# Kernel tuning notes

Hardware: AMD Instinct MI355X
Metric: run time of the kernel (lower is better)

Reference implementation:

```python
import jax, jax.numpy as jnp
import numpy as np

N, E, D, L, H = 100000, 1600000, 64, 4, 4
C = D // H  # head dim = 16
NEG_SLOPE = 0.2


def layer_norm(x, g, b, eps=1e-5):
    m = jnp.mean(x, axis=-1, keepdims=True)
    v = jnp.var(x, axis=-1, keepdims=True)
    return (x - m) * jax.lax.rsqrt(v + eps) * g + b


def setup_inputs() -> dict:
    key = jax.random.key(0)
    ks = jax.random.split(key, 12)
    node_feats = jax.random.normal(ks[0], (N, D), jnp.float32)
    edge_feats = jax.random.normal(ks[1], (E, D), jnp.float32)
    edge_index = jax.random.randint(ks[2], (2, E), 0, N, jnp.int32)
    s = 0.1
    conv_w = jax.random.normal(ks[3], (L, D, H * C), jnp.float32) * s
    att_src = jax.random.normal(ks[4], (L, H, C), jnp.float32) * s
    att_dst = jax.random.normal(ks[5], (L, H, C), jnp.float32) * s
    edge_w = jax.random.normal(ks[6], (L, D, H * C), jnp.float32) * s
    att_edge = jax.random.normal(ks[7], (L, H, C), jnp.float32) * s
    conv_b = jnp.zeros((L, D), jnp.float32)
    ln_g = jnp.ones((L, D), jnp.float32)
    ln_b = jnp.zeros((L, D), jnp.float32)
    Din = 3 * D  # edge-update MLP input dim (node_i, node_j, edge)
    up1_w = jax.random.normal(ks[8], (L, Din, Din), jnp.float32) * 0.05
    up1_b = jnp.zeros((L, Din), jnp.float32)
    up_ln_g = jnp.ones((L, Din), jnp.float32)
    up_ln_b = jnp.zeros((L, Din), jnp.float32)
    up2_w = jax.random.normal(ks[9], (L, Din, D), jnp.float32) * 0.05
    up2_b = jnp.zeros((L, D), jnp.float32)
    return dict(node_feats=node_feats, edge_feats=edge_feats, edge_index=edge_index,
                conv_w=conv_w, att_src=att_src, att_dst=att_dst, edge_w=edge_w,
                att_edge=att_edge, conv_b=conv_b, ln_g=ln_g, ln_b=ln_b,
                up1_w=up1_w, up1_b=up1_b, up_ln_g=up_ln_g, up_ln_b=up_ln_b,
                up2_w=up2_w, up2_b=up2_b)


def _gat_conv(x, e, src, dst, w, a_s, a_d, ew, a_e, b):
    n = x.shape[0]
    # add self loops with zero edge attr
    loop = jnp.arange(n, dtype=src.dtype)
    src_f = jnp.concatenate([src, loop])
    dst_f = jnp.concatenate([dst, loop])
    xh = (x @ w).reshape(n, H, C)                       # [N,H,C]
    alpha_src = jnp.einsum('nhc,hc->nh', xh, a_s)        # [N,H]
    alpha_dst = jnp.einsum('nhc,hc->nh', xh, a_d)
    eh = (e @ ew).reshape(-1, H, C)                      # [E,H,C]
    alpha_edge = jnp.einsum('ehc,hc->eh', eh, a_e)       # [E,H]
    alpha_edge = jnp.concatenate([alpha_edge, jnp.zeros((n, H), x.dtype)])
    alpha = alpha_src[src_f] + alpha_dst[dst_f] + alpha_edge  # [E+N,H]
    alpha = jax.nn.leaky_relu(alpha, NEG_SLOPE)
    # segment softmax over destination neighborhoods
    amax = jax.ops.segment_max(alpha, dst_f, num_segments=n)
    alpha = jnp.exp(alpha - amax[dst_f])
    asum = jax.ops.segment_sum(alpha, dst_f, num_segments=n)
    alpha = alpha / (asum[dst_f] + 1e-16)
    msg = xh[src_f] * alpha[:, :, None]                  # [E+N,H,C]
    out = jax.ops.segment_sum(msg.reshape(-1, H * C), dst_f, num_segments=n)
    return out + b


def _edge_update(nf, ef, src, dst, w1, b1, g, bg, w2, b2):
    x = jnp.concatenate([nf[src], nf[dst], ef], axis=-1)  # [E,3D]
    h = layer_norm(x @ w1 + b1, g, bg)
    h = jax.nn.relu(h)
    return h @ w2 + b2 + ef


def reference(node_feats, edge_feats, edge_index, conv_w, att_src, att_dst,
              edge_w, att_edge, conv_b, ln_g, ln_b, up1_w, up1_b,
              up_ln_g, up_ln_b, up2_w, up2_b):
    src, dst = edge_index[0], edge_index[1]
    nf, ef = node_feats, edge_feats
    for l in range(L):
        conv = _gat_conv(nf, ef, src, dst, conv_w[l], att_src[l], att_dst[l],
                         edge_w[l], att_edge[l], conv_b[l])
        conv = layer_norm(conv, ln_g[l], ln_b[l])
        nf = jax.nn.relu(conv) + nf  # dropout in eval mode = identity
        ef = _edge_update(nf, ef, src, dst, up1_w[l], up1_b[l],
                          up_ln_g[l], up_ln_b[l], up2_w[l], up2_b[l])
    return nf, ef
```

## Files before the change

### kernel.cpp

```cpp
#include <hip/hip_runtime.h>
#include <math.h>

#define NN 100000
#define NE 1600000
#define DD 64
#define NL 4
#define NH 4
#define NC 16
#define DIN 192
#define SLOPE 0.2f
#define EB 64
#define XSTR 200
#define FSTR 66
#define RSTR 68
#define LOG2E 1.44269504088896340736f

typedef __bf16 bf8 __attribute__((ext_vector_type(8)));
typedef __bf16 bf4 __attribute__((ext_vector_type(4)));
typedef __bf16 bf2 __attribute__((ext_vector_type(2)));
typedef float f32x4 __attribute__((ext_vector_type(4)));

__device__ __forceinline__ f32x4 MFMA(bf8 a, bf8 b, f32x4 c) {
  return __builtin_amdgcn_mfma_f32_16x16x32_bf16(a, b, c, 0, 0, 0);
}

__global__ void k_pack_w1(const float* __restrict__ W1, __bf16* __restrict__ WH) {
  int gidx = blockIdx.x * 256 + threadIdx.x;
  if (gidx >= 4 * 4608) return;
  int lyr = gidx / 4608, rem = gidx % 4608;
  int lane = rem & 63, ts = rem >> 6;
  int s = ts % 6, t = ts / 6;
  const float* Wl = W1 + (size_t)lyr * DIN * DIN;
  size_t base = (size_t)lyr * 36864 + ((size_t)(t * 6 + s) * 64 + lane) * 8;
  int k0 = s * 32 + (lane >> 4) * 8, n = t * 16 + (lane & 15);
#pragma unroll
  for (int j = 0; j < 8; ++j)
    WH[base + j] = (__bf16)Wl[(size_t)(k0 + j) * DIN + n];
}

__global__ void k_pack_w2(const float* __restrict__ W2, __bf16* __restrict__ WH) {
  int gidx = blockIdx.x * 256 + threadIdx.x;
  if (gidx >= 4 * 1536) return;
  int lyr = gidx / 1536, rem = gidx % 1536;
  int lane = rem & 63, ts = rem >> 6;
  int s = ts % 6, t = ts / 6;
  const float* Wl = W2 + (size_t)lyr * DIN * DD;
  size_t base = (size_t)lyr * 12288 + ((size_t)(t * 6 + s) * 64 + lane) * 8;
  int k0 = s * 32 + (lane >> 4) * 8, n = t * 16 + (lane & 15);
#pragma unroll
  for (int j = 0; j < 8; ++j)
    WH[base + j] = (__bf16)Wl[(size_t)(k0 + j) * DD + n];
}

__global__ void k_w2v(const float* __restrict__ up2_w, const float* __restrict__ up2_b,
                      const float* __restrict__ vbuf, __bf16* __restrict__ W2VP,
                      __bf16* __restrict__ VP, float* __restrict__ bvdot) {
  int l = blockIdx.x;
  const float* vn = vbuf + (l + 1) * 256;
  int t = threadIdx.x;
  if (t < 384) {
    int s = t >> 6, lane = t & 63;
    int i = lane & 15, k0 = s * 32 + (lane >> 4) * 8;
    const float* W2 = up2_w + (size_t)l * DIN * DD;
    __bf16* out = W2VP + (size_t)l * 3072 + ((size_t)(s * 64 + lane)) * 8;
#pragma unroll
    for (int j = 0; j < 8; ++j) {
      float val = 0.f;
      if (i < 4)
        for (int n = 0; n < DD; ++n)
          val = fmaf(W2[(size_t)(k0 + j) * DD + n], vn[n * NH + i], val);
      out[j] = (__bf16)val;
    }
  }
  if (t < 128) {
    int s2 = t >> 6, lane = t & 63;
    int i = lane & 15, k0 = s2 * 32 + (lane >> 4) * 8;
    __bf16* out = VP + (size_t)l * 1024 + ((size_t)(s2 * 64 + lane)) * 8;
#pragma unroll
    for (int j = 0; j < 8; ++j)
      out[j] = (i < 4) ? (__bf16)vn[(k0 + j) * NH + i] : (__bf16)0.f;
  }
  if (t < 4) {
    const float* b2 = up2_b + (size_t)l * DD;
    float bv = 0.f;
    for (int n = 0; n < DD; ++n) bv = fmaf(b2[n], vn[n * NH + t], bv);
    bvdot[l * 4 + t] = bv;
  }
}

__global__ void k_zero(int* __restrict__ deg) {
  int i = blockIdx.x * 256 + threadIdx.x;
  if (i < NN) deg[i] = 0;
}

__global__ void k_hist(const int* __restrict__ dst, int* __restrict__ deg) {
  int e = blockIdx.x * 256 + threadIdx.x;
  if (e < NE) atomicAdd(&deg[dst[e]], 1);
}

__global__ void k_scan1(const int* __restrict__ deg, int* __restrict__ offs,
                        int* __restrict__ bsum) {
  __shared__ int sh[256];
  int t = threadIdx.x, b = blockIdx.x;
  int i0 = b * 1024 + t * 4;
  int d0 = (i0 + 0 < NN) ? deg[i0 + 0] : 0;
  int d1 = (i0 + 1 < NN) ? deg[i0 + 1] : 0;
  int d2 = (i0 + 2 < NN) ? deg[i0 + 2] : 0;
  int d3 = (i0 + 3 < NN) ? deg[i0 + 3] : 0;
  int s4 = d0 + d1 + d2 + d3;
  sh[t] = s4;
  __syncthreads();
  int p = 0;
#pragma unroll
  for (int off = 1; off < 256; off <<= 1) {
    int v = (t >= off) ? sh[t - off] : 0;
    __syncthreads();
    sh[t] += v;
    __syncthreads();
  }
  p = sh[t] - s4;
  if (t == 255) bsum[b] = sh[255];
  if (i0 + 0 < NN) offs[i0 + 0] = p;
  if (i0 + 1 < NN) offs[i0 + 1] = p + d0;
  if (i0 + 2 < NN) offs[i0 + 2] = p + d0 + d1;
  if (i0 + 3 < NN) offs[i0 + 3] = p + d0 + d1 + d2;
}

__global__ void k_scan2(int* __restrict__ bsum, int* __restrict__ boff,
                        int* __restrict__ offs, int nb) {
  if (threadIdx.x == 0 && blockIdx.x == 0) {
    int run = 0;
    for (int k = 0; k < nb; ++k) { boff[k] = run; run += bsum[k]; }
    offs[NN] = NE;
  }
}

__global__ void k_scan3(int* __restrict__ offs, const int* __restrict__ boff,
                        int* __restrict__ cursor) {
  int i = blockIdx.x * 256 + threadIdx.x;
  if (i < NN) {
    int v = offs[i] + boff[i >> 10];
    offs[i] = v;
    cursor[i] = v;
  }
}

__global__ void k_scatter(const int* __restrict__ src, const int* __restrict__ dst,
                          int* __restrict__ cursor, int* __restrict__ csr_src,
                          int* __restrict__ csr_eid) {
  int e = blockIdx.x * 256 + threadIdx.x;
  if (e >= NE) return;
  int pos = atomicAdd(&cursor[dst[e]], 1);
  csr_src[pos] = src[e];
  csr_eid[pos] = e;
}

__global__ void k_v_all(const float* __restrict__ ew_all, const float* __restrict__ ae_all,
                        float* __restrict__ vbuf) {
  int l = blockIdx.x;
  const float* ew = ew_all + (size_t)l * DD * DD;
  const float* ae = ae_all + (size_t)l * NH * NC;
  int d = threadIdx.x >> 2, h = threadIdx.x & 3;
  float s = 0.f;
#pragma unroll
  for (int c = 0; c < NC; ++c) s = fmaf(ew[d * DD + h * NC + c], ae[h * NC + c], s);
  vbuf[l * 256 + d * NH + h] = s;
}

__global__ void k_init_nf(const float* __restrict__ node_feats, float* __restrict__ nf) {
  int i = blockIdx.x * 256 + threadIdx.x;
  if (i < NN * DD) nf[i] = node_feats[i];
}

__global__ void k_xh(const float* __restrict__ nf, const float* __restrict__ W,
                     const float* __restrict__ as_, const float* __restrict__ ad_,
                     __bf16* __restrict__ xh16, float* __restrict__ asrc,
                     float* __restrict__ adst) {
  int t = blockIdx.x * 4 + (threadIdx.x >> 6);
  int d = threadIdx.x & 63;
  if (t >= NN) return;
  const float* x = nf + (size_t)t * DD;
  float acc = 0.f;
#pragma unroll
  for (int k = 0; k < DD; ++k) acc = fmaf(x[k], W[k * DD + d], acc);
  xh16[(size_t)t * DD + d] = (__bf16)acc;
  int h = d >> 4, c = d & 15;
  float ps = acc * as_[h * NC + c];
  float pd = acc * ad_[h * NC + c];
#pragma unroll
  for (int off = 8; off >= 1; off >>= 1) {
    ps += __shfl_xor(ps, off, 64);
    pd += __shfl_xor(pd, off, 64);
  }
  if (c == 0) { asrc[t * NH + h] = ps; adst[t * NH + h] = pd; }
}

__global__ void k_pass1f(const float* __restrict__ edge_feats,
                         const float* __restrict__ v,
                         __bf16* __restrict__ ef16, float* __restrict__ araw) {
  int e = blockIdx.x * 64 + (threadIdx.x >> 2);
  int part = threadIdx.x & 3;
  if (e >= NE) return;
  float ph0 = 0.f, ph1 = 0.f, ph2 = 0.f, ph3 = 0.f;
  const float4* ep = (const float4*)(edge_feats + (size_t)e * DD + part * 16);
  const float4* v4 = (const float4*)v;
  bf4 outv[4];
#pragma unroll
  for (int c4 = 0; c4 < 4; ++c4) {
    float4 x = ep[c4];
    outv[c4][0] = (__bf16)x.x; outv[c4][1] = (__bf16)x.y;
    outv[c4][2] = (__bf16)x.z; outv[c4][3] = (__bf16)x.w;
    int d0 = part * 16 + c4 * 4;
    float4 va = v4[d0], vb = v4[d0 + 1], vc = v4[d0 + 2], vd = v4[d0 + 3];
    ph0 = fmaf(x.x, va.x, fmaf(x.y, vb.x, fmaf(x.z, vc.x, fmaf(x.w, vd.x, ph0))));
    ph1 = fmaf(x.x, va.y, fmaf(x.y, vb.y, fmaf(x.z, vc.y, fmaf(x.w, vd.y, ph1))));
    ph2 = fmaf(x.x, va.z, fmaf(x.y, vb.z, fmaf(x.z, vc.z, fmaf(x.w, vd.z, ph2))));
    ph3 = fmaf(x.x, va.w, fmaf(x.y, vb.w, fmaf(x.z, vc.w, fmaf(x.w, vd.w, ph3))));
  }
  *(bf8*)&ef16[(size_t)e * DD + part * 16] =
      (bf8){outv[0][0], outv[0][1], outv[0][2], outv[0][3],
            outv[1][0], outv[1][1], outv[1][2], outv[1][3]};
  *(bf8*)&ef16[(size_t)e * DD + part * 16 + 8] =
      (bf8){outv[2][0], outv[2][1], outv[2][2], outv[2][3],
            outv[3][0], outv[3][1], outv[3][2], outv[3][3]};
#pragma unroll
  for (int off = 1; off <= 2; off <<= 1) {
    ph0 += __shfl_xor(ph0, off, 64);
    ph1 += __shfl_xor(ph1, off, 64);
    ph2 += __shfl_xor(ph2, off, 64);
    ph3 += __shfl_xor(ph3, off, 64);
  }
  float pe = (part == 0) ? ph0 : (part == 1) ? ph1 : (part == 2) ? ph2 : ph3;
  araw[(size_t)e * NH + part] = pe;
}

__global__ __launch_bounds__(256) void k_gather3(
    const __bf16* __restrict__ xh16, const float* __restrict__ araw,
    const int* __restrict__ csr_src, const int* __restrict__ csr_eid,
    const int* __restrict__ offs,
    const float* __restrict__ asrc, const float* __restrict__ adst,
    const float* __restrict__ cb, const float* __restrict__ g,
    const float* __restrict__ bln, float* __restrict__ nf,
    __bf16* __restrict__ nf16) {
  int t = blockIdx.x * 4 + (threadIdx.x >> 6);
  int d = threadIdx.x & 63;
  if (t >= NN) return;
  int h = d >> 4;
  int o0 = offs[t], o1 = offs[t + 1];
  int deg = o1 - o0;
  float adh = adst[t * NH + h];

  float sh = asrc[t * NH + h] + adh;
  sh = ((sh > 0.f) ? sh : SLOPE * sh) * LOG2E;
  float m_run = sh;
  float wsum = 1.f;
  float acc = (float)xh16[(size_t)t * DD + d];

  int j = 0;
  for (; j + 1 < deg; j += 2) {
    int pos0 = o0 + j, pos1 = o0 + j + 1;
    int sp0 = csr_src[pos0], sp1 = csr_src[pos1];
    int e0i = csr_eid[pos0], e1i = csr_eid[pos1];
    float ar0 = asrc[sp0 * NH + h] + adh + araw[(size_t)e0i * NH + h];
    float ar1 = asrc[sp1 * NH + h] + adh + araw[(size_t)e1i * NH + h];
    ar0 = ((ar0 > 0.f) ? ar0 : SLOPE * ar0) * LOG2E;
    ar1 = ((ar1 > 0.f) ? ar1 : SLOPE * ar1) * LOG2E;
    float x0 = (float)xh16[(size_t)sp0 * DD + d];
    float x1 = (float)xh16[(size_t)sp1 * DD + d];
    float mnew = fmaxf(m_run, fmaxf(ar0, ar1));
    float rold = exp2f(m_run - mnew);
    float w0 = exp2f(ar0 - mnew), w1 = exp2f(ar1 - mnew);
    acc = fmaf(w1, x1, fmaf(w0, x0, acc * rold));
    wsum = fmaf(w0 + w1, 1.f, wsum * rold);
    m_run = mnew;
  }
  if (j < deg) {
    int pos = o0 + j;
    int sp = csr_src[pos];
    int ei = csr_eid[pos];
    float ar = asrc[sp * NH + h] + adh + araw[(size_t)ei * NH + h];
    ar = ((ar > 0.f) ? ar : SLOPE * ar) * LOG2E;
    float xv = (float)xh16[(size_t)sp * DD + d];
    float mnew = fmaxf(m_run, ar);
    float rold = exp2f(m_run - mnew);
    float w = exp2f(ar - mnew);
    acc = fmaf(w, xv, acc * rold);
    wsum = fmaf(w, 1.f, wsum * rold);
    m_run = mnew;
  }

  float val = acc / (wsum + 1e-16f) + cb[d];
  float m = val;
#pragma unroll
  for (int off = 32; off >= 1; off >>= 1) m += __shfl_xor(m, off, 64);
  m *= (1.f / 64.f);
  float c = val - m;
  float q = c * c;
#pragma unroll
  for (int off = 32; off >= 1; off >>= 1) q += __shfl_xor(q, off, 64);
  float rstd = 1.f / sqrtf(q * (1.f / 64.f) + 1e-5f);
  float y = c * rstd * g[d] + bln[d];
  y = fmaxf(y, 0.f);
  float out = y + nf[(size_t)t * DD + d];
  nf[(size_t)t * DD + d] = out;
  nf16[(size_t)t * DD + d] = (__bf16)out;
}

__global__ __launch_bounds__(256, 4) void k_edge_mlp15(
    const __bf16* __restrict__ nf16, __bf16* __restrict__ ef16,
    float* __restrict__ efout,
    const int* __restrict__ src, const int* __restrict__ dst,
    const __bf16* __restrict__ W1H, const float* __restrict__ b1,
    const float* __restrict__ g, const float* __restrict__ bg,
    const __bf16* __restrict__ W2H, const float* __restrict__ b2,
    const __bf16* __restrict__ W2VP, const __bf16* __restrict__ VP,
    const float* __restrict__ bvdot, float* __restrict__ araw, int last) {
  __shared__ __bf16 XH[EB * XSTR];
  __shared__ __bf16 RESB[EB * RSTR];
  __shared__ __bf16 Pb[EB * 8];
  int tid = threadIdx.x;
  int e0 = blockIdx.x * EB;
  float* XF = (float*)XH;

  {
    int row = tid >> 2, p = tid & 3;
    int se = src[e0 + row], de = dst[e0 + row];
    const bf8* psrc = (const bf8*)(nf16 + (size_t)se * DD + p * 16);
    *(bf8*)&XH[row * XSTR + p * 16]     = psrc[0];
    *(bf8*)&XH[row * XSTR + p * 16 + 8] = psrc[1];
    const bf8* pdst = (const bf8*)(nf16 + (size_t)de * DD + p * 16);
    *(bf8*)&XH[row * XSTR + 64 + p * 16]     = pdst[0];
    *(bf8*)&XH[row * XSTR + 64 + p * 16 + 8] = pdst[1];
    const bf8* pef = (const bf8*)(ef16 + (size_t)(e0 + row) * DD + p * 16);
    bf8 ev0 = pef[0], ev1 = pef[1];
    *(bf8*)&XH[row * XSTR + 128 + p * 16]     = ev0;
    *(bf8*)&XH[row * XSTR + 128 + p * 16 + 8] = ev1;
    *(bf8*)&RESB[row * RSTR + p * 16]     = ev0;
    *(bf8*)&RESB[row * RSTR + p * 16 + 8] = ev1;
  }
  __syncthreads();

  int cg = tid >> 6, l = tid & 63;
  int gq = l >> 4, i = l & 15;
  int col = cg * 16 + i;

  f32x4 acc[4][3];
#pragma unroll
  for (int rt = 0; rt < 4; ++rt)
#pragma unroll
    for (int t = 0; t < 3; ++t) acc[rt][t] = (f32x4){0.f, 0.f, 0.f, 0.f};
  f32x4 accP = (f32x4){0.f, 0.f, 0.f, 0.f};
  f32x4 accQ = (f32x4){0.f, 0.f, 0.f, 0.f};

#pragma unroll
  for (int s = 0; s < 6; ++s) {
    bf8 a[4];
#pragma unroll
    for (int rt = 0; rt < 4; ++rt)
      a[rt] = *(const bf8*)&XH[(rt * 16 + i) * XSTR + s * 32 + gq * 8];
#pragma unroll
    for (int t = 0; t < 3; ++t) {
      bf8 bh = *(const bf8*)(W1H + ((size_t)((cg * 3 + t) * 6 + s) * 64 + l) * 8);
#pragma unroll
      for (int rt = 0; rt < 4; ++rt) acc[rt][t] = MFMA(a[rt], bh, acc[rt][t]);
    }
    if (!last && s >= 4) {
      bf8 acg = *(const bf8*)&XH[(cg * 16 + i) * XSTR + s * 32 + gq * 8];
      bf8 vp = *(const bf8*)(VP + ((size_t)((s - 4) * 64 + l)) * 8);
      accP = MFMA(acg, vp, accP);
    }
  }

  float b1v[3], gv[3], bgv[3];
#pragma unroll
  for (int t = 0; t < 3; ++t) {
    int n = cg * 48 + t * 16 + i;
    b1v[t] = b1[n]; gv[t] = g[n]; bgv[t] = bg[n];
  }
#pragma unroll
  for (int rt = 0; rt < 4; ++rt)
#pragma unroll
    for (int t = 0; t < 3; ++t)
#pragma unroll
      for (int r = 0; r < 4; ++r) acc[rt][t][r] += b1v[t];

#pragma unroll
  for (int rt = 0; rt < 4; ++rt)
#pragma unroll
    for (int r = 0; r < 4; ++r) {
      float sm = 0.f, sq = 0.f;
#pragma unroll
      for (int t = 0; t < 3; ++t) { float x = acc[rt][t][r]; sm += x; sq = fmaf(x, x, sq); }
#pragma unroll
      for (int off = 1; off <= 8; off <<= 1) {
        sm += __shfl_xor(sm, off, 64);
        sq += __shfl_xor(sq, off, 64);
      }
      if (i == 0) {
        int row = rt * 16 + gq * 4 + r;
        bf2 pr; pr[0] = (__bf16)sm; pr[1] = (__bf16)sq;
        *(bf2*)&Pb[row * 8 + cg * 2] = pr;
      }
    }
  __syncthreads();

  if (tid < EB) {
    bf8 pv = *(const bf8*)&Pb[tid * 8];
    float sm = (float)pv[0] + (float)pv[2] + (float)pv[4] + (float)pv[6];
    float sq = (float)pv[1] + (float)pv[3] + (float)pv[5] + (float)pv[7];
    float mean = sm * (1.f / (float)DIN);
    float var = sq * (1.f / (float)DIN) - mean * mean;
    float rstd = 1.f / sqrtf(var + 1e-5f);
    bf2 mv; mv[0] = (__bf16)mean; mv[1] = (__bf16)rstd;
    *(bf2*)&Pb[tid * 8] = mv;
  }
  __syncthreads();

#pragma unroll
  for (int rt = 0; rt < 4; ++rt)
#pragma unroll
    for (int r = 0; r < 4; ++r) {
      int row = rt * 16 + gq * 4 + r;
      bf2 mv = *(const bf2*)&Pb[row * 8];
      float mean = (float)mv[0], rstd = (float)mv[1];
#pragma unroll
      for (int t = 0; t < 3; ++t) {
        float y = (acc[rt][t][r] - mean) * rstd * gv[t] + bgv[t];
        y = fmaxf(y, 0.f);
        XH[row * XSTR + cg * 48 + t * 16 + i] = (__bf16)y;
      }
    }
  __syncthreads();

  f32x4 acc2[4];
#pragma unroll
  for (int rt = 0; rt < 4; ++rt) acc2[rt] = (f32x4){0.f, 0.f, 0.f, 0.f};

#pragma unroll
  for (int s = 0; s < 6; ++s) {
    bf8 a2[4];
#pragma unroll
    for (int rt = 0; rt < 4; ++rt)
      a2[rt] = *(const bf8*)&XH[(rt * 16 + i) * XSTR + s * 32 + gq * 8];
    bf8 bh = *(const bf8*)(W2H + ((size_t)(cg * 6 + s) * 64 + l) * 8);
#pragma unroll
    for (int rt = 0; rt < 4; ++rt) acc2[rt] = MFMA(a2[rt], bh, acc2[rt]);
    if (!last) {
      bf8 acg = *(const bf8*)&XH[(cg * 16 + i) * XSTR + s * 32 + gq * 8];
      bf8 wv = *(const bf8*)(W2VP + ((size_t)(s * 64 + l)) * 8);
      accQ = MFMA(acg, wv, accQ);
    }
  }
  __syncthreads();

  float b2v = b2[col];
#pragma unroll
  for (int rt = 0; rt < 4; ++rt)
#pragma unroll
    for (int r = 0; r < 4; ++r) {
      int row = rt * 16 + gq * 4 + r;
      float resv = (float)RESB[row * RSTR + col];
      XF[row * FSTR + col] = acc2[rt][r] + b2v + resv;
    }

  if (!last && i < 4) {
    float bvd = bvdot[i];
#pragma unroll
    for (int r = 0; r < 4; ++r) {
      int row = cg * 16 + gq * 4 + r;
      araw[(size_t)(e0 + row) * NH + i] = accP[r] + accQ[r] + bvd;
    }
  }
  __syncthreads();

  {
    int row = tid >> 2, q = tid & 3;
    const float* fr = &XF[row * FSTR + q * 16];
    if (last) {
      float* op = efout + (size_t)(e0 + row) * DD + q * 16;
#pragma unroll
      for (int k = 0; k < 4; ++k)
        *(float4*)(op + k * 4) = *(const float4*)(fr + k * 4);
    } else {
      bf8 o0, o1;
#pragma unroll
      for (int k = 0; k < 8; ++k) { o0[k] = (__bf16)fr[k]; o1[k] = (__bf16)fr[k + 8]; }
      __bf16* op = ef16 + (size_t)(e0 + row) * DD + q * 16;
      *(bf8*)op = o0;
      *(bf8*)(op + 8) = o1;
    }
  }
}

extern "C" void kernel_launch(void* const* d_in, const int* in_sizes, int n_in,
                              void* d_out, int out_size, void* d_ws, size_t ws_size,
                              hipStream_t stream) {
  const float* node_feats = (const float*)d_in[0];
  const float* edge_feats = (const float*)d_in[1];
  const int*   edge_index = (const int*)d_in[2];
  const float* conv_w  = (const float*)d_in[3];
  const float* att_src = (const float*)d_in[4];
  const float* att_dst = (const float*)d_in[5];
  const float* edge_w  = (const float*)d_in[6];
  const float* att_edge= (const float*)d_in[7];
  const float* conv_b  = (const float*)d_in[8];
  const float* ln_g    = (const float*)d_in[9];
  const float* ln_b    = (const float*)d_in[10];
  const float* up1_w   = (const float*)d_in[11];
  const float* up1_b   = (const float*)d_in[12];
  const float* up_ln_g = (const float*)d_in[13];
  const float* up_ln_b = (const float*)d_in[14];
  const float* up2_w   = (const float*)d_in[15];
  const float* up2_b   = (const float*)d_in[16];

  const int* src = edge_index;
  const int* dst = edge_index + NE;

  float* nf = (float*)d_out;
  float* efout = nf + (size_t)NN * DD;

  float* w = (float*)d_ws;
  __bf16* xh16 = (__bf16*)w; w += (size_t)NN * DD / 2;
  __bf16* nf16 = (__bf16*)w; w += (size_t)NN * DD / 2;
  __bf16* ef16 = (__bf16*)w; w += (size_t)NE * DD / 2;
  float* asrc  = w; w += (size_t)NN * NH;
  float* adst  = w; w += (size_t)NN * NH;
  float* araw  = w; w += (size_t)NE * NH;
  float* vbuf  = w; w += 4 * 256;
  float* bvdot = w; w += 16;
  __bf16* W1H  = (__bf16*)w; w += (size_t)4 * 36864 / 2;
  __bf16* W2H  = (__bf16*)w; w += (size_t)4 * 12288 / 2;
  __bf16* W2VP = (__bf16*)w; w += (size_t)3 * 3072 / 2;
  __bf16* VPb  = (__bf16*)w; w += (size_t)3 * 1024 / 2;
  int* deg     = (int*)w; w += NN;
  int* offs    = (int*)w; w += NN + 1;
  int* cursor  = (int*)w; w += NN;
  int* bsum    = (int*)w; w += 128;
  int* boff    = (int*)w; w += 128;
  int* csr_src = (int*)w; w += NE;
  int* csr_eid = (int*)w; w += NE;

  k_init_nf<<<(NN * DD + 255) / 256, 256, 0, stream>>>(node_feats, nf);
  k_pack_w1<<<72, 256, 0, stream>>>(up1_w, W1H);
  k_pack_w2<<<24, 256, 0, stream>>>(up2_w, W2H);

  const int nb = (NN + 1023) / 1024;
  k_zero<<<(NN + 255) / 256, 256, 0, stream>>>(deg);
  k_hist<<<(NE + 255) / 256, 256, 0, stream>>>(dst, deg);
  k_scan1<<<nb, 256, 0, stream>>>(deg, offs, bsum);
  k_scan2<<<1, 64, 0, stream>>>(bsum, boff, offs, nb);
  k_scan3<<<(NN + 255) / 256, 256, 0, stream>>>(offs, boff, cursor);
  k_scatter<<<(NE + 255) / 256, 256, 0, stream>>>(src, dst, cursor, csr_src, csr_eid);

  k_v_all<<<4, 256, 0, stream>>>(edge_w, att_edge, vbuf);
  k_w2v<<<3, 384, 0, stream>>>(up2_w, up2_b, vbuf, W2VP, VPb, bvdot);
  k_pass1f<<<NE / 64, 256, 0, stream>>>(edge_feats, vbuf, ef16, araw);

  for (int l = 0; l < NL; ++l) {
    int last = (l == NL - 1) ? 1 : 0;
    k_xh<<<NN / 4, 256, 0, stream>>>(nf, conv_w + (size_t)l * DD * DD,
                                     att_src + (size_t)l * NH * NC,
                                     att_dst + (size_t)l * NH * NC, xh16, asrc, adst);
    k_gather3<<<NN / 4, 256, 0, stream>>>(xh16, araw, csr_src, csr_eid, offs,
                                          asrc, adst,
                                          conv_b + (size_t)l * DD,
                                          ln_g + (size_t)l * DD,
                                          ln_b + (size_t)l * DD, nf, nf16);
    k_edge_mlp15<<<NE / EB, 256, 0, stream>>>(
        nf16, ef16, efout, src, dst,
        W1H + (size_t)l * 36864, up1_b + (size_t)l * DIN,
        up_ln_g + (size_t)l * DIN, up_ln_b + (size_t)l * DIN,
        W2H + (size_t)l * 12288, up2_b + (size_t)l * DD,
        last ? W2VP : (W2VP + (size_t)l * 3072),
        last ? VPb : (VPb + (size_t)l * 1024),
        bvdot + (size_t)l * 4, araw, last);
  }
}
```

Before: 2.789 ms.

## Fuse next-layer node projection into gather kernel, keep node residual in bf16

Removes the separate per-layer k_xh launch by computing the next layer's projection, xh and attention logits at the end of the gather kernel. The input row is broadcast across lanes with shuffles, and xh and the attention buffers are double-buffered across layers. The fp32 node-feature copy and init kernel are dropped: the residual is now carried in bf16 and fp32 is written only on the last layer. This saves node-feature traffic and launches, at the cost of bf16 rounding accumulating in the residual across layers.

```diff
diff --git a/kernel.cpp b/kernel.cpp
--- a/kernel.cpp
+++ b/kernel.cpp
@@ -167,19 +167,15 @@
   vbuf[l * 256 + d * NH + h] = s;
 }
 
-__global__ void k_init_nf(const float* __restrict__ node_feats, float* __restrict__ nf) {
-  int i = blockIdx.x * 256 + threadIdx.x;
-  if (i < NN * DD) nf[i] = node_feats[i];
-}
-
-__global__ void k_xh(const float* __restrict__ nf, const float* __restrict__ W,
-                     const float* __restrict__ as_, const float* __restrict__ ad_,
-                     __bf16* __restrict__ xh16, float* __restrict__ asrc,
-                     float* __restrict__ adst) {
+__global__ void k_xh0(const float* __restrict__ node_feats, const float* __restrict__ W,
+                      const float* __restrict__ as_, const float* __restrict__ ad_,
+                      __bf16* __restrict__ nf16, __bf16* __restrict__ xh16,
+                      float* __restrict__ asrc, float* __restrict__ adst) {
   int t = blockIdx.x * 4 + (threadIdx.x >> 6);
   int d = threadIdx.x & 63;
   if (t >= NN) return;
-  const float* x = nf + (size_t)t * DD;
+  const float* x = node_feats + (size_t)t * DD;
+  nf16[(size_t)t * DD + d] = (__bf16)x[d];
   float acc = 0.f;
 #pragma unroll
   for (int k = 0; k < DD; ++k) acc = fmaf(x[k], W[k * DD + d], acc);
@@ -234,14 +230,17 @@
   araw[(size_t)e * NH + part] = pe;
 }
 
-__global__ __launch_bounds__(256) void k_gather3(
+__global__ __launch_bounds__(256) void k_gather4(
     const __bf16* __restrict__ xh16, const float* __restrict__ araw,
     const int* __restrict__ csr_src, const int* __restrict__ csr_eid,
     const int* __restrict__ offs,
     const float* __restrict__ asrc, const float* __restrict__ adst,
     const float* __restrict__ cb, const float* __restrict__ g,
-    const float* __restrict__ bln, float* __restrict__ nf,
-    __bf16* __restrict__ nf16) {
+    const float* __restrict__ bln, __bf16* __restrict__ nf16,
+    float* __restrict__ nfout,
+    const float* __restrict__ Wn, const float* __restrict__ asn,
+    const float* __restrict__ adn, __bf16* __restrict__ xh16n,
+    float* __restrict__ asrcn, float* __restrict__ adstn, int last) {
   int t = blockIdx.x * 4 + (threadIdx.x >> 6);
   int d = threadIdx.x & 63;
   if (t >= NN) return;
@@ -301,9 +300,29 @@
   float rstd = 1.f / sqrtf(q * (1.f / 64.f) + 1e-5f);
   float y = c * rstd * g[d] + bln[d];
   y = fmaxf(y, 0.f);
-  float out = y + nf[(size_t)t * DD + d];
-  nf[(size_t)t * DD + d] = out;
+  float out = y + (float)nf16[(size_t)t * DD + d];
   nf16[(size_t)t * DD + d] = (__bf16)out;
+
+  if (last) {
+    nfout[(size_t)t * DD + d] = out;
+  } else {
+    float acc2 = 0.f;
+#pragma unroll 8
+    for (int k = 0; k < DD; ++k) {
+      float xk = __shfl(out, k, 64);
+      acc2 = fmaf(xk, Wn[k * DD + d], acc2);
+    }
+    xh16n[(size_t)t * DD + d] = (__bf16)acc2;
+    int cc = d & 15;
+    float ps = acc2 * asn[h * NC + cc];
+    float pd = acc2 * adn[h * NC + cc];
+#pragma unroll
+    for (int off = 8; off >= 1; off >>= 1) {
+      ps += __shfl_xor(ps, off, 64);
+      pd += __shfl_xor(pd, off, 64);
+    }
+    if (cc == 0) { asrcn[t * NH + h] = ps; adstn[t * NH + h] = pd; }
+  }
 }
 
 __global__ __launch_bounds__(256, 4) void k_edge_mlp15(
@@ -520,11 +539,14 @@
   float* efout = nf + (size_t)NN * DD;
 
   float* w = (float*)d_ws;
-  __bf16* xh16 = (__bf16*)w; w += (size_t)NN * DD / 2;
+  __bf16* xh16a = (__bf16*)w; w += (size_t)NN * DD / 2;
+  __bf16* xh16b = (__bf16*)w; w += (size_t)NN * DD / 2;
   __bf16* nf16 = (__bf16*)w; w += (size_t)NN * DD / 2;
   __bf16* ef16 = (__bf16*)w; w += (size_t)NE * DD / 2;
-  float* asrc  = w; w += (size_t)NN * NH;
-  float* adst  = w; w += (size_t)NN * NH;
+  float* asA   = w; w += (size_t)NN * NH;
+  float* adA   = w; w += (size_t)NN * NH;
+  float* asB   = w; w += (size_t)NN * NH;
+  float* adB   = w; w += (size_t)NN * NH;
   float* araw  = w; w += (size_t)NE * NH;
   float* vbuf  = w; w += 4 * 256;
   float* bvdot = w; w += 16;
@@ -540,7 +562,10 @@
   int* csr_src = (int*)w; w += NE;
   int* csr_eid = (int*)w; w += NE;
 
-  k_init_nf<<<(NN * DD + 255) / 256, 256, 0, stream>>>(node_feats, nf);
+  __bf16* xh[2] = {xh16a, xh16b};
+  float* as_[2] = {asA, asB};
+  float* ad_[2] = {adA, adB};
+
   k_pack_w1<<<72, 256, 0, stream>>>(up1_w, W1H);
   k_pack_w2<<<24, 256, 0, stream>>>(up2_w, W2H);
 
@@ -554,18 +579,21 @@
 
   k_v_all<<<4, 256, 0, stream>>>(edge_w, att_edge, vbuf);
   k_w2v<<<3, 384, 0, stream>>>(up2_w, up2_b, vbuf, W2VP, VPb, bvdot);
+  k_xh0<<<NN / 4 + 1, 256, 0, stream>>>(node_feats, conv_w, att_src, att_dst,
+                                        nf16, xh16a, asA, adA);
   k_pass1f<<<NE / 64, 256, 0, stream>>>(edge_feats, vbuf, ef16, araw);
 
   for (int l = 0; l < NL; ++l) {
     int last = (l == NL - 1) ? 1 : 0;
-    k_xh<<<NN / 4, 256, 0, stream>>>(nf, conv_w + (size_t)l * DD * DD,
-                                     att_src + (size_t)l * NH * NC,
-                                     att_dst + (size_t)l * NH * NC, xh16, asrc, adst);
-    k_gather3<<<NN / 4, 256, 0, stream>>>(xh16, araw, csr_src, csr_eid, offs,
-                                          asrc, adst,
-                                          conv_b + (size_t)l * DD,
-                                          ln_g + (size_t)l * DD,
-                                          ln_b + (size_t)l * DD, nf, nf16);
+    int cur = l & 1, nxt = (l + 1) & 1;
+    k_gather4<<<NN / 4 + 1, 256, 0, stream>>>(
+        xh[cur], araw, csr_src, csr_eid, offs, as_[cur], ad_[cur],
+        conv_b + (size_t)l * DD, ln_g + (size_t)l * DD, ln_b + (size_t)l * DD,
+        nf16, nf,
+        last ? conv_w : (conv_w + (size_t)(l + 1) * DD * DD),
+        last ? att_src : (att_src + (size_t)(l + 1) * NH * NC),
+        last ? att_dst : (att_dst + (size_t)(l + 1) * NH * NC),
+        xh[nxt], as_[nxt], ad_[nxt], last);
     k_edge_mlp15<<<NE / EB, 256, 0, stream>>>(
         nf16, ef16, efout, src, dst,
         W1H + (size_t)l * 36864, up1_b + (size_t)l * DIN,
```

Measured after the change: 2.643 ms. 1.06x faster.
